# Kernel optimization log

Measured on AMD Instinct MI355X. Metric: run time of the kernel, lower is better.

Reference implementation:

```python
import jax, jax.numpy as jnp
import numpy as np
import math

B, H, S, D = 2, 8, 2048, 64

def setup_inputs() -> dict:
    key = jax.random.key(0)
    kq, kk, kv = jax.random.split(key, 3)
    q = jax.random.normal(kq, (B, H, S, D), dtype=jnp.float32)
    k = jax.random.normal(kk, (B, H, S, D), dtype=jnp.float32)
    v = jax.random.normal(kv, (B, H, S, D), dtype=jnp.float32)
    # causal mask: True means masked (filled with -1e9), matching masked_fill
    mask = jnp.triu(jnp.ones((S, S), dtype=jnp.bool_), k=1)
    return {"q": q, "k": k, "v": v, "mask": mask}

def reference(q, k, v, mask) -> jnp.ndarray:
    d_model = q.shape[-1]
    # [..., s, t] scores
    att = jnp.einsum('bhsd,bhtd->bhst', q, k) / math.sqrt(d_model)
    if mask is not None:
        # broadcast mask over leading dims; True -> -1e9
        att = jnp.where(mask, jnp.float32(-1e9), att)
    # numerically stable softmax over last axis (matches manual Softmax)
    att = jax.nn.softmax(att, axis=-1)
    return jnp.einsum('bhst,bhtd->bhsd', att, v)
```

## Files before the change

### kernel.cpp

```cpp
#include <hip/hip_runtime.h>

typedef __bf16 bf16x8 __attribute__((ext_vector_type(8)));
typedef float  f32x16 __attribute__((ext_vector_type(16)));

constexpr int Sn  = 2048;
constexpr int Dh  = 64;
constexpr int QT  = 32;
constexpr int KVT = 32;
constexpr int NBH = 16;
constexpr int NT  = Sn / QT;
constexpr int NW  = 4;
constexpr int TSTR = 4 * 64 * 8;

constexpr float SCL = 0.125f * 1.44269504088896340736f;

constexpr size_t ELEMS  = (size_t)NBH * Sn * Dh;
constexpr size_t QB_OFF = 0;
constexpr size_t KP_OFF = ELEMS;
constexpr size_t VP_OFF = 2 * ELEMS;
constexpr size_t WS_NEED = 3 * ELEMS * 2;

__device__ inline bf16x8 cvt8(float4 a, float4 b, float s) {
  bf16x8 r;
  r[0] = (__bf16)(a.x * s); r[1] = (__bf16)(a.y * s);
  r[2] = (__bf16)(a.z * s); r[3] = (__bf16)(a.w * s);
  r[4] = (__bf16)(b.x * s); r[5] = (__bf16)(b.y * s);
  r[6] = (__bf16)(b.z * s); r[7] = (__bf16)(b.w * s);
  return r;
}

__global__ __launch_bounds__(256) void prep(
    const float* __restrict__ q, const float* __restrict__ k,
    const float* __restrict__ v, __bf16* __restrict__ ws)
{
  __shared__ float tl[KVT][Dh + 1];
  const int g    = blockIdx.x;
  const int tid  = threadIdx.x;
  const int wv   = tid >> 6;
  const int lane = tid & 63;
  const int hi   = lane >> 5;
  const int ln   = lane & 31;
  const size_t tbase = (size_t)g * (KVT * Dh);

  {
    const float* qp = q + tbase + (size_t)tid * 8;
    const float4 a = *(const float4*)qp;
    const float4 b = *(const float4*)(qp + 4);
    *(bf16x8*)(ws + QB_OFF + tbase + (size_t)tid * 8) = cvt8(a, b, SCL);
  }
  {
    const float* kp = k + tbase;
#pragma unroll
    for (int e = 0; e < 2; ++e) {
      const int i4  = tid + e * 256;
      const float4 x = *(const float4*)(kp + (size_t)i4 * 4);
      const int row = i4 >> 4, col = (i4 & 15) * 4;
      tl[row][col] = x.x; tl[row][col + 1] = x.y;
      tl[row][col + 2] = x.z; tl[row][col + 3] = x.w;
    }
  }
  __syncthreads();
  {
    bf16x8 r;
#pragma unroll
    for (int i = 0; i < 8; ++i) r[i] = (__bf16)tl[ln][16 * wv + 8 * hi + i];
    *(bf16x8*)(ws + KP_OFF + ((size_t)(g * 4 + wv) * 64 + lane) * 8) = r;
  }
  __syncthreads();
  {
    const float* vp = v + tbase;
#pragma unroll
    for (int e = 0; e < 2; ++e) {
      const int i4  = tid + e * 256;
      const float4 x = *(const float4*)(vp + (size_t)i4 * 4);
      const int row = i4 >> 4, col = (i4 & 15) * 4;
      tl[row][col] = x.x; tl[row][col + 1] = x.y;
      tl[row][col + 2] = x.z; tl[row][col + 3] = x.w;
    }
  }
  __syncthreads();
  {
    const int dt = wv >> 1, T = wv & 1;
    bf16x8 r;
#pragma unroll
    for (int i = 0; i < 8; ++i) {
      const int row = 16 * T + 4 * hi + (i & 3) + 8 * (i >> 2);
      r[i] = (__bf16)tl[row][32 * dt + ln];
    }
    *(bf16x8*)(ws + VP_OFF + ((size_t)(g * 4 + wv) * 64 + lane) * 8) = r;
  }
}

#define LOADKV(K0,K1,K2,K3,V0,V1,V2,V3,kt_) do {                         \
    const __bf16* kp_ = kpB + (size_t)(kt_) * TSTR + lane * 8;           \
    K0 = *(const bf16x8*)(kp_);                                          \
    K1 = *(const bf16x8*)(kp_ + 512);                                    \
    K2 = *(const bf16x8*)(kp_ + 1024);                                   \
    K3 = *(const bf16x8*)(kp_ + 1536);                                   \
    const __bf16* vp_ = vpB + (size_t)(kt_) * TSTR + lane * 8;           \
    V0 = *(const bf16x8*)(vp_);                                          \
    V1 = *(const bf16x8*)(vp_ + 512);                                    \
    V2 = *(const bf16x8*)(vp_ + 1024);                                   \
    V3 = *(const bf16x8*)(vp_ + 1536);                                   \
  } while (0)

#define COMPUTE_NM(K0,K1,K2,K3,V0,V1,V2,V3) do {                         \
    f32x16 st;                                                           \
    _Pragma("unroll")                                                    \
    for (int i_ = 0; i_ < 16; ++i_) st[i_] = 0.f;                        \
    st = __builtin_amdgcn_mfma_f32_32x32x16_bf16(K0, qf[0], st, 0, 0, 0);\
    st = __builtin_amdgcn_mfma_f32_32x32x16_bf16(K1, qf[1], st, 0, 0, 0);\
    st = __builtin_amdgcn_mfma_f32_32x32x16_bf16(K2, qf[2], st, 0, 0, 0);\
    st = __builtin_amdgcn_mfma_f32_32x32x16_bf16(K3, qf[3], st, 0, 0, 0);\
    float p[16];                                                         \
    _Pragma("unroll")                                                    \
    for (int r_ = 0; r_ < 16; ++r_) p[r_] = __builtin_amdgcn_exp2f(st[r_]); \
    bf16x8 pa0, pa1;                                                     \
    _Pragma("unroll")                                                    \
    for (int i_ = 0; i_ < 8; ++i_) { pa0[i_] = (__bf16)p[i_]; pa1[i_] = (__bf16)p[8 + i_]; } \
    o0 = __builtin_amdgcn_mfma_f32_32x32x16_bf16(pa0, V0, o0, 0, 0, 0);  \
    o1 = __builtin_amdgcn_mfma_f32_32x32x16_bf16(pa0, V2, o1, 0, 0, 0);  \
    ls = __builtin_amdgcn_mfma_f32_32x32x16_bf16(pa0, ONESV, ls, 0, 0, 0);\
    o0 = __builtin_amdgcn_mfma_f32_32x32x16_bf16(pa1, V1, o0, 0, 0, 0);  \
    o1 = __builtin_amdgcn_mfma_f32_32x32x16_bf16(pa1, V3, o1, 0, 0, 0);  \
    ls = __builtin_amdgcn_mfma_f32_32x32x16_bf16(pa1, ONESV, ls, 0, 0, 0);\
  } while (0)

#define COMPUTE_MS(K0,K1,K2,K3,V0,V1,V2,V3) do {                         \
    f32x16 st;                                                           \
    _Pragma("unroll")                                                    \
    for (int i_ = 0; i_ < 16; ++i_) st[i_] = 0.f;                        \
    st = __builtin_amdgcn_mfma_f32_32x32x16_bf16(K0, qf[0], st, 0, 0, 0);\
    st = __builtin_amdgcn_mfma_f32_32x32x16_bf16(K1, qf[1], st, 0, 0, 0);\
    st = __builtin_amdgcn_mfma_f32_32x32x16_bf16(K2, qf[2], st, 0, 0, 0);\
    st = __builtin_amdgcn_mfma_f32_32x32x16_bf16(K3, qf[3], st, 0, 0, 0);\
    _Pragma("unroll")                                                    \
    for (int r_ = 0; r_ < 16; ++r_) {                                    \
      const int tl_ = (r_ & 3) + 8 * (r_ >> 2) + 4 * hi;                 \
      if (tl_ > ln) st[r_] = -1e30f;                                     \
    }                                                                    \
    float p[16];                                                         \
    _Pragma("unroll")                                                    \
    for (int r_ = 0; r_ < 16; ++r_) p[r_] = __builtin_amdgcn_exp2f(st[r_]); \
    bf16x8 pa0, pa1;                                                     \
    _Pragma("unroll")                                                    \
    for (int i_ = 0; i_ < 8; ++i_) { pa0[i_] = (__bf16)p[i_]; pa1[i_] = (__bf16)p[8 + i_]; } \
    o0 = __builtin_amdgcn_mfma_f32_32x32x16_bf16(pa0, V0, o0, 0, 0, 0);  \
    o1 = __builtin_amdgcn_mfma_f32_32x32x16_bf16(pa0, V2, o1, 0, 0, 0);  \
    ls = __builtin_amdgcn_mfma_f32_32x32x16_bf16(pa0, ONESV, ls, 0, 0, 0);\
    o0 = __builtin_amdgcn_mfma_f32_32x32x16_bf16(pa1, V1, o0, 0, 0, 0);  \
    o1 = __builtin_amdgcn_mfma_f32_32x32x16_bf16(pa1, V3, o1, 0, 0, 0);  \
    ls = __builtin_amdgcn_mfma_f32_32x32x16_bf16(pa1, ONESV, ls, 0, 0, 0);\
  } while (0)

__global__ __launch_bounds__(256) void attn_bf16(
    const __bf16* __restrict__ ws, float* __restrict__ og)
{
  __shared__ __bf16 ldsO[NW][QT][Dh];
  __shared__ float  ldsL[NW][QT];

  const int b    = blockIdx.x;
  const int bh   = 2 * (b & 7) + ((b >> 3) & 1);
  const int tile = 63 - (b >> 4);
  const int tid  = threadIdx.x;
  const int w    = tid >> 6;
  const int lane = tid & 63;
  const int hi   = lane >> 5;
  const int ln   = lane & 31;

  const __bf16* qB  = ws + QB_OFF + (size_t)bh * Sn * Dh;
  const __bf16* kpB = ws + KP_OFF + (size_t)bh * NT * TSTR;
  const __bf16* vpB = ws + VP_OFF + (size_t)bh * NT * TSTR;

  bf16x8 ONESV;
#pragma unroll
  for (int i = 0; i < 8; ++i) ONESV[i] = (__bf16)1.0f;

  bf16x8 qf[4];
  {
    const __bf16* qp = qB + ((size_t)(tile * QT + ln)) * Dh + 8 * hi;
#pragma unroll
    for (int c = 0; c < 4; ++c) qf[c] = *(const bf16x8*)(qp + 16 * c);
  }

  f32x16 o0, o1, ls;
#pragma unroll
  for (int i = 0; i < 16; ++i) { o0[i] = 0.f; o1[i] = 0.f; ls[i] = 0.f; }

  bf16x8 kA0, kA1, kA2, kA3, vA0, vA1, vA2, vA3;
  bf16x8 kB0, kB1, kB2, kB3, vB0, vB1, vB2, vB3;

  int kt = w;
  while (kt + NW < tile) {
    LOADKV(kA0,kA1,kA2,kA3,vA0,vA1,vA2,vA3, kt);
    LOADKV(kB0,kB1,kB2,kB3,vB0,vB1,vB2,vB3, kt + NW);
    COMPUTE_NM(kA0,kA1,kA2,kA3,vA0,vA1,vA2,vA3);
    COMPUTE_NM(kB0,kB1,kB2,kB3,vB0,vB1,vB2,vB3);
    kt += 2 * NW;
  }
  if (kt < tile) {
    LOADKV(kA0,kA1,kA2,kA3,vA0,vA1,vA2,vA3, kt);
    COMPUTE_NM(kA0,kA1,kA2,kA3,vA0,vA1,vA2,vA3);
    kt += NW;
  }
  if (kt == tile) {
    LOADKV(kA0,kA1,kA2,kA3,vA0,vA1,vA2,vA3, tile);
    COMPUTE_MS(kA0,kA1,kA2,kA3,vA0,vA1,vA2,vA3);
  }

#pragma unroll
  for (int r = 0; r < 16; ++r) {
    const int rl = (r & 3) + 8 * (r >> 2) + 4 * hi;
    ldsO[w][rl][ln]      = (__bf16)o0[r];
    ldsO[w][rl][32 + ln] = (__bf16)o1[r];
    if (ln == 0) ldsL[w][rl] = ls[r];
  }
  __syncthreads();

#pragma unroll
  for (int e = 0; e < 8; ++e) {
    const int i   = e * 256 + tid;
    const int row = i >> 6;
    const int col = i & 63;
    float L = 0.f, o = 0.f;
#pragma unroll
    for (int wv = 0; wv < NW; ++wv) {
      L += ldsL[wv][row];
      o += (float)ldsO[wv][row][col];
    }
    og[((size_t)bh * Sn + tile * QT + row) * Dh + col] = o / L;
  }
}

__global__ __launch_bounds__(256) void attn_f32(
    const float* __restrict__ qg, const float* __restrict__ kg,
    const float* __restrict__ vg, float* __restrict__ og)
{
  __shared__ float ldsO[4][QT][Dh];
  __shared__ float ldsM[4][QT];
  __shared__ float ldsL[4][QT];

  const int g    = blockIdx.x;
  const int bh   = g >> 6;
  const int idx  = g & 63;
  const int tile = (idx & 1) ? (63 - (idx >> 1)) : (idx >> 1);
  const int w    = threadIdx.x >> 6;
  const int lane = threadIdx.x & 63;
  const int hi   = lane >> 5;
  const int ln   = lane & 31;

  const size_t base = (size_t)bh * Sn * Dh;
  const float* Q = qg + base;
  const float* K = kg + base;
  const float* V = vg + base;
  float*       O = og + base;
  const int srow = tile * QT + ln;

  bf16x8 qf[4];
  {
    const float* qp = Q + (size_t)srow * Dh + 8 * hi;
#pragma unroll
    for (int c = 0; c < 4; ++c) {
      const float4 x = *(const float4*)(qp + 16 * c);
      const float4 y = *(const float4*)(qp + 16 * c + 4);
      qf[c] = cvt8(x, y, 0.125f);
    }
  }
  f32x16 o0, o1;
#pragma unroll
  for (int i = 0; i < 16; ++i) { o0[i] = 0.f; o1[i] = 0.f; }
  float m = -1e30f, lsum = 0.f;

  for (int kt = w; kt <= tile; kt += 4) {
    const int t0 = kt * KVT;
    bf16x8 kf[4];
    const float* kp = K + (size_t)(t0 + ln) * Dh + 8 * hi;
#pragma unroll
    for (int c = 0; c < 4; ++c) {
      const float4 x = *(const float4*)(kp + 16 * c);
      const float4 y = *(const float4*)(kp + 16 * c + 4);
      kf[c] = cvt8(x, y, 1.0f);
    }
    f32x16 st;
#pragma unroll
    for (int i = 0; i < 16; ++i) st[i] = 0.f;
#pragma unroll
    for (int c = 0; c < 4; ++c)
      st = __builtin_amdgcn_mfma_f32_32x32x16_bf16(kf[c], qf[c], st, 0, 0, 0);
    if (kt == tile) {
#pragma unroll
      for (int r = 0; r < 16; ++r) {
        const int tl = (r & 3) + 8 * (r >> 2) + 4 * hi;
        if (tl > ln) st[r] = -1e30f;
      }
    }
    float tmax = st[0];
#pragma unroll
    for (int r = 1; r < 16; ++r) tmax = fmaxf(tmax, st[r]);
    tmax = fmaxf(tmax, __shfl_xor(tmax, 32));
    const float mnew = fmaxf(m, tmax);
    const bool  resc = __any(mnew > m);
    const float corr = __expf(m - mnew);
    m = mnew;
    float p[16];
    float psum = 0.f;
#pragma unroll
    for (int r = 0; r < 16; ++r) { p[r] = __expf(st[r] - mnew); psum += p[r]; }
    psum += __shfl_xor(psum, 32);
    lsum = lsum * corr + psum;
    if (resc) {
#pragma unroll
      for (int r = 0; r < 16; ++r) {
        const float cr = __shfl(corr, (r & 3) + 8 * (r >> 2) + 4 * hi);
        o0[r] *= cr; o1[r] *= cr;
      }
    }
    bf16x8 pa0, pa1;
#pragma unroll
    for (int i = 0; i < 8; ++i) { pa0[i] = (__bf16)p[i]; pa1[i] = (__bf16)p[8 + i]; }
#pragma unroll
    for (int T = 0; T < 2; ++T) {
      const int tb = t0 + 16 * T + 4 * hi;
      bf16x8 vb0, vb1;
#pragma unroll
      for (int j = 0; j < 4; ++j) {
        const float* vp  = V + (size_t)(tb + j) * Dh + ln;
        const float* vp2 = V + (size_t)(tb + 8 + j) * Dh + ln;
        vb0[j]     = (__bf16)vp[0];
        vb1[j]     = (__bf16)vp[32];
        vb0[4 + j] = (__bf16)vp2[0];
        vb1[4 + j] = (__bf16)vp2[32];
      }
      const bf16x8 pa = T ? pa1 : pa0;
      o0 = __builtin_amdgcn_mfma_f32_32x32x16_bf16(pa, vb0, o0, 0, 0, 0);
      o1 = __builtin_amdgcn_mfma_f32_32x32x16_bf16(pa, vb1, o1, 0, 0, 0);
    }
  }
#pragma unroll
  for (int r = 0; r < 16; ++r) {
    const int rl = (r & 3) + 8 * (r >> 2) + 4 * hi;
    ldsO[w][rl][ln]      = o0[r];
    ldsO[w][rl][32 + ln] = o1[r];
  }
  if (hi == 0) { ldsM[w][ln] = m; ldsL[w][ln] = lsum; }
  __syncthreads();
  const int tid = threadIdx.x;
#pragma unroll
  for (int e = 0; e < 8; ++e) {
    const int i   = e * 256 + tid;
    const int row = i >> 6;
    const int col = i & 63;
    const float m0 = ldsM[0][row], m1 = ldsM[1][row], m2 = ldsM[2][row], m3 = ldsM[3][row];
    const float M  = fmaxf(fmaxf(m0, m1), fmaxf(m2, m3));
    const float e0 = __expf(m0 - M), e1 = __expf(m1 - M), e2 = __expf(m2 - M), e3 = __expf(m3 - M);
    const float L  = ldsL[0][row] * e0 + ldsL[1][row] * e1 + ldsL[2][row] * e2 + ldsL[3][row] * e3;
    const float o  = ldsO[0][row][col] * e0 + ldsO[1][row][col] * e1
                   + ldsO[2][row][col] * e2 + ldsO[3][row][col] * e3;
    O[(size_t)(tile * QT + row) * Dh + col] = o / L;
  }
}

extern "C" void kernel_launch(void* const* d_in, const int* in_sizes, int n_in,
                              void* d_out, int out_size, void* d_ws, size_t ws_size,
                              hipStream_t stream) {
  const float* q = (const float*)d_in[0];
  const float* k = (const float*)d_in[1];
  const float* v = (const float*)d_in[2];
  float* out = (float*)d_out;
  if (ws_size >= WS_NEED) {
    prep<<<dim3(NBH * NT), dim3(256), 0, stream>>>(q, k, v, (__bf16*)d_ws);
    attn_bf16<<<dim3(NBH * NT), dim3(256), 0, stream>>>((const __bf16*)d_ws, out);
  } else {
    attn_f32<<<dim3(1024), dim3(256), 0, stream>>>(q, k, v, out);
  }
}
```

Baseline: 31.96 us.

## Software-pipeline K/V register loads with triple-buffered rolling prefetch

Replaces the load-two-then-compute-two loop with a three-stage rolling register pipeline. Each buffer is refilled with the K/V tile three steps ahead right after it is consumed, so global loads overlap the MFMA work of the other two buffers. The cost is a third set of bf16x8 K/V registers, which may raise VGPR pressure and lower occupancy. It also adds more complex tail handling for the remaining iterations.

```diff
diff --git a/kernel.cpp b/kernel.cpp
--- a/kernel.cpp
+++ b/kernel.cpp
@@ -189,21 +189,39 @@
 
   bf16x8 kA0, kA1, kA2, kA3, vA0, vA1, vA2, vA3;
   bf16x8 kB0, kB1, kB2, kB3, vB0, vB1, vB2, vB3;
-
+  bf16x8 kC0, kC1, kC2, kC3, vC0, vC1, vC2, vC3;
+
+  const int n = (tile > w) ? ((tile - 1 - w) / NW + 1) : 0;
   int kt = w;
-  while (kt + NW < tile) {
-    LOADKV(kA0,kA1,kA2,kA3,vA0,vA1,vA2,vA3, kt);
-    LOADKV(kB0,kB1,kB2,kB3,vB0,vB1,vB2,vB3, kt + NW);
+  if (n >= 1) LOADKV(kA0,kA1,kA2,kA3,vA0,vA1,vA2,vA3, kt);
+  if (n >= 2) LOADKV(kB0,kB1,kB2,kB3,vB0,vB1,vB2,vB3, kt + NW);
+  if (n >= 3) LOADKV(kC0,kC1,kC2,kC3,vC0,vC1,vC2,vC3, kt + 2 * NW);
+
+  int i = 0;
+  while (i + 6 <= n) {
     COMPUTE_NM(kA0,kA1,kA2,kA3,vA0,vA1,vA2,vA3);
+    LOADKV(kA0,kA1,kA2,kA3,vA0,vA1,vA2,vA3, kt + 3 * NW);
     COMPUTE_NM(kB0,kB1,kB2,kB3,vB0,vB1,vB2,vB3);
-    kt += 2 * NW;
-  }
-  if (kt < tile) {
-    LOADKV(kA0,kA1,kA2,kA3,vA0,vA1,vA2,vA3, kt);
+    LOADKV(kB0,kB1,kB2,kB3,vB0,vB1,vB2,vB3, kt + 4 * NW);
+    COMPUTE_NM(kC0,kC1,kC2,kC3,vC0,vC1,vC2,vC3);
+    LOADKV(kC0,kC1,kC2,kC3,vC0,vC1,vC2,vC3, kt + 5 * NW);
+    kt += 3 * NW;
+    i  += 3;
+  }
+  const int rem = n - i;
+  if (rem >= 1) {
     COMPUTE_NM(kA0,kA1,kA2,kA3,vA0,vA1,vA2,vA3);
-    kt += NW;
-  }
-  if (kt == tile) {
+    if (rem >= 4) LOADKV(kA0,kA1,kA2,kA3,vA0,vA1,vA2,vA3, kt + 3 * NW);
+  }
+  if (rem >= 2) {
+    COMPUTE_NM(kB0,kB1,kB2,kB3,vB0,vB1,vB2,vB3);
+    if (rem >= 5) LOADKV(kB0,kB1,kB2,kB3,vB0,vB1,vB2,vB3, kt + 4 * NW);
+  }
+  if (rem >= 3) COMPUTE_NM(kC0,kC1,kC2,kC3,vC0,vC1,vC2,vC3);
+  if (rem >= 4) COMPUTE_NM(kA0,kA1,kA2,kA3,vA0,vA1,vA2,vA3);
+  if (rem >= 5) COMPUTE_NM(kB0,kB1,kB2,kB3,vB0,vB1,vB2,vB3);
+
+  if ((tile & (NW - 1)) == w) {
     LOADKV(kA0,kA1,kA2,kA3,vA0,vA1,vA2,vA3, tile);
     COMPUTE_MS(kA0,kA1,kA2,kA3,vA0,vA1,vA2,vA3);
   }
@@ -219,9 +237,9 @@
 
 #pragma unroll
   for (int e = 0; e < 8; ++e) {
-    const int i   = e * 256 + tid;
-    const int row = i >> 6;
-    const int col = i & 63;
+    const int i2  = e * 256 + tid;
+    const int row = i2 >> 6;
+    const int col = i2 & 63;
     float L = 0.f, o = 0.f;
 #pragma unroll
     for (int wv = 0; wv < NW; ++wv) {
```

Result: no change. 31.73 us (-0.7%).
